# Optimization experiments

Measured on AMD Instinct MI355X. Metric: run time of the kernel, lower is better.

## Reference

```python
import jax, jax.numpy as jnp
import numpy as np


def setup_inputs() -> dict:
    key = jax.random.key(0)
    k1, k2, k3, k4, k5, k6 = jax.random.split(key, 6)
    B, S, I, H = 64, 512, 1024, 1024
    scale_ih = 1.0 / np.sqrt(I)
    scale_hh = 1.0 / np.sqrt(H)
    return {
        "inputs": jax.random.normal(k1, (B, S, I), dtype=jnp.float32),
        "h0": jax.random.normal(k2, (1, B, H), dtype=jnp.float32),
        "weight_ih": jax.random.normal(k3, (H, I), dtype=jnp.float32) * scale_ih,
        "weight_hh": jax.random.normal(k4, (H, H), dtype=jnp.float32) * scale_hh,
        "bias_ih": jax.random.normal(k5, (H,), dtype=jnp.float32) * 0.01,
        "bias_hh": jax.random.normal(k6, (H,), dtype=jnp.float32) * 0.01,
    }


def reference(inputs, h0, weight_ih, weight_hh, bias_ih, bias_hh):
    # Elman RNN with ReLU: h_t = relu(x_t W_ih^T + b_ih + h_{t-1} W_hh^T + b_hh)
    # inputs: [B, S, I]; h0: [1, B, H]
    # Precompute the input projection for all timesteps in one big GEMM.
    x_proj = jnp.einsum('bsi,hi->bsh', inputs, weight_ih) + bias_ih + bias_hh  # [B,S,H]

    def step(h, xp_t):
        h_new = jax.nn.relu(xp_t + jnp.matmul(h, weight_hh.T))  # [B,H]
        return h_new, h_new

    h_init = h0[0]  # [B, H]
    h_last, outs = jax.lax.scan(step, h_init, jnp.swapaxes(x_proj, 0, 1))  # outs: [S,B,H]
    outputs = jnp.swapaxes(outs, 0, 1)  # [B, S, H]
    h_n = h_last[None]  # [1, B, H]
    return outputs, h_n
```

## Files before the change

### kernel.cpp

```cpp
#include <hip/hip_runtime.h>
#include <hip/hip_bf16.h>
#include <stdint.h>

#define BATCH 64
#define SEQ   512
#define INDIM 1024
#define HDIM  1024
#define NBLK  256
#define NGRP  8
#define GSLOT 32
#define FPAD  16
#define HELEMS 32768

typedef short bf16x8 __attribute__((ext_vector_type(8)));
typedef short s16x4  __attribute__((ext_vector_type(4)));
typedef float f32x4  __attribute__((ext_vector_type(4)));
typedef unsigned short u16;
typedef unsigned int   u32;
typedef u32 u32x2 __attribute__((ext_vector_type(2)));
typedef u32 u32x4 __attribute__((ext_vector_type(4)));
typedef u16 u16x4 __attribute__((ext_vector_type(4)));

static __device__ __forceinline__ u16 f2bf(float x) {
  unsigned int u = __float_as_uint(x);
  u += 0x7fffu + ((u >> 16) & 1u);
  return (u16)(u >> 16);
}
static __device__ __forceinline__ float bf2f(u16 b) {
  return __uint_as_float(((unsigned int)b) << 16);
}

static __device__ __forceinline__ int coh_ld_i32(const int* p) {
  int v;
  asm volatile("global_load_dword %0, %1, off sc0 sc1\n\t"
               "s_waitcnt vmcnt(0)"
               : "=&v"(v) : "v"(p) : "memory");
  return v;
}

static __device__ __forceinline__ void split4(float4 v, u16x4& hi, u16x4& lo) {
  hi.x = f2bf(v.x); lo.x = f2bf(v.x - bf2f(hi.x));
  hi.y = f2bf(v.y); lo.y = f2bf(v.y - bf2f(hi.y));
  hi.z = f2bf(v.z); lo.z = f2bf(v.z - bf2f(hi.z));
  hi.w = f2bf(v.w); lo.w = f2bf(v.w - bf2f(hi.w));
}
static __device__ __forceinline__ bf16x8 ld8(const u16* p) {
  s16x4 a = *(const s16x4*)p;
  s16x4 b = *(const s16x4*)(p + 4);
  return __builtin_shufflevector(a, b, 0, 1, 2, 3, 4, 5, 6, 7);
}

__global__ void init0(u32* __restrict__ ws, int n) {
  int i = blockIdx.x * blockDim.x + threadIdx.x;
  if (i < n) ws[i] = 0;
}

__global__ void init1(const float* __restrict__ h0, u16* __restrict__ hbase) {
  int i = blockIdx.x * blockDim.x + threadIdx.x;
  if (i < BATCH * HDIM) {
    int b = i >> 10, k = i & 1023;
    int g = b >> 3, r = b & 7;
    int k32 = k >> 5, kg = (k >> 3) & 3, j = k & 7;
    float x = h0[i];
    u16 h = f2bf(x);
    size_t u = (size_t)(g * 2) * HELEMS + ((size_t)(k32 * 4 + kg) * 16 + r) * 16 + j;
    hbase[u] = h;
    hbase[u + 8] = f2bf(x - bf2f(h));
  }
}

__global__ __launch_bounds__(256) void xproj_kernel(const float* __restrict__ A,
                                                    const float* __restrict__ W,
                                                    const float* __restrict__ bih,
                                                    const float* __restrict__ bhh,
                                                    float* __restrict__ C) {
  __shared__ u16 Ah[4][128][12], Al[4][128][12], Bh[4][128][12], Bl[4][128][12];
  const int nb = blockIdx.x;
  const int mb = blockIdx.y;
  const int m_base = mb * 128, n_base = nb * 128;
  const int tid = (int)threadIdx.x;
  const int wid = tid >> 6, lane = tid & 63;
  const int wm = wid >> 1, wn = wid & 1;
  const int r = lane & 15, kg = lane >> 4;
  const int srow = tid >> 1;
  const int skq  = (tid & 1) * 16;

  const float* ap0 = A + (size_t)(m_base + srow) * INDIM + skq;
  const float* bp0 = W + (size_t)(n_base + srow) * INDIM + skq;

  f32x4 acc[4][4] = {};

  for (int k0 = 0; k0 < INDIM; k0 += 32) {
    float4 av[4], bv[4];
#pragma unroll
    for (int i = 0; i < 4; ++i) {
      av[i] = *(const float4*)(ap0 + k0 + i * 4);
      bv[i] = *(const float4*)(bp0 + k0 + i * 4);
    }
    __syncthreads();
#pragma unroll
    for (int i = 0; i < 4; ++i) {
      int kk = skq + i * 4;
      int kgw = kk >> 3, off = kk & 7;
      u16x4 hi, lo;
      split4(av[i], hi, lo);
      *(u16x4*)&Ah[kgw][srow][off] = hi;
      *(u16x4*)&Al[kgw][srow][off] = lo;
      split4(bv[i], hi, lo);
      *(u16x4*)&Bh[kgw][srow][off] = hi;
      *(u16x4*)&Bl[kgw][srow][off] = lo;
    }
    __syncthreads();

    bf16x8 ah[4], al[4], bhv[4], blv[4];
#pragma unroll
    for (int mf = 0; mf < 4; ++mf) {
      int row = wm * 64 + mf * 16 + r;
      ah[mf] = ld8(&Ah[kg][row][0]);
      al[mf] = ld8(&Al[kg][row][0]);
    }
#pragma unroll
    for (int nf = 0; nf < 4; ++nf) {
      int row = wn * 64 + nf * 16 + r;
      bhv[nf] = ld8(&Bh[kg][row][0]);
      blv[nf] = ld8(&Bl[kg][row][0]);
    }
#pragma unroll
    for (int mf = 0; mf < 4; ++mf)
#pragma unroll
      for (int nf = 0; nf < 4; ++nf) {
        acc[mf][nf] = __builtin_amdgcn_mfma_f32_16x16x32_bf16(ah[mf], bhv[nf], acc[mf][nf], 0, 0, 0);
        acc[mf][nf] = __builtin_amdgcn_mfma_f32_16x16x32_bf16(ah[mf], blv[nf], acc[mf][nf], 0, 0, 0);
        acc[mf][nf] = __builtin_amdgcn_mfma_f32_16x16x32_bf16(al[mf], bhv[nf], acc[mf][nf], 0, 0, 0);
      }
  }

#pragma unroll
  for (int nf = 0; nf < 4; ++nf) {
    int col = n_base + wn * 64 + nf * 16 + r;
    float bias = bih[col] + bhh[col];
#pragma unroll
    for (int mf = 0; mf < 4; ++mf) {
      int rowb = m_base + wm * 64 + mf * 16 + kg * 4;
#pragma unroll
      for (int q = 0; q < 4; ++q) {
        C[(size_t)(rowb + q) * HDIM + col] = acc[mf][nf][q] + bias;
      }
    }
  }
}

__global__ __launch_bounds__(512, 1) void rnn_scan(
    const float* __restrict__ Whh, float* __restrict__ out,
    u16* hbase, int* flags) {
  __shared__ u16 WH[32][2][64][8], WL[32][2][64][8];
  __shared__ __align__(16) float red[2][8][2][8][20];

  const int blk = (int)blockIdx.x;
  const int grp = blk & 7;
  const int slot = blk >> 3;
  const int n0 = slot * 32;
  const int tid = (int)threadIdx.x;
  const int wv = tid >> 6, lane = tid & 63;
  const int r = lane & 15, kg = lane >> 4;

  for (int it = 0; it < 16; ++it) {
    int f4 = it * 512 + tid;
    int row = f4 >> 8;
    int k0 = (f4 & 255) * 4;
    float4 v = *(const float4*)(Whh + (size_t)(n0 + row) * HDIM + k0);
    int k32 = k0 >> 5, kgg = (k0 >> 3) & 3, j = k0 & 7;
    int nt = row >> 4, ln = kgg * 16 + (row & 15);
    u16x4 hi, lo;
    split4(v, hi, lo);
    *(u16x4*)&WH[k32][nt][ln][j] = hi;
    *(u16x4*)&WL[k32][nt][ln][j] = lo;
  }
  __syncthreads();

  u16* const hb[2] = {hbase + (size_t)(grp * 2) * HELEMS,
                      hbase + (size_t)(grp * 2 + 1) * HELEMS};
  int* const gflag = flags + grp * GSLOT * FPAD;
  const bool zrow = (lane & 15) >= 8;
  const int* const pollp = gflag + (wv * 4 + (lane & 3)) * FPAD;

  const int erow = lane >> 3;
  const int ec = lane & 7;
  const float* xp0 = out + ((size_t)(grp * 8 + erow) * SEQ) * HDIM + n0 + ec * 4;
  float4 xf;
  if (wv == 0) xf = *(const float4*)xp0;

  for (int t = 0; t < SEQ; ++t) {
    const int p = t & 1;
    const u16* hc = hb[p];
    u16* hn = hb[p ^ 1];

    if (t > 0) {
      int v;
      do { v = coh_ld_i32(pollp); } while (!__all(v >= t));
    }

    u32x4 hh[4], hl[4];
    if (!zrow) {
      const char* a0 = (const char*)hc + ((size_t)(wv * 4) * 64 + lane) * 32;
      const char* a1 = a0 + 4096;
      asm volatile(
          "global_load_dwordx4 %0, %8, off sc0 sc1\n\t"
          "global_load_dwordx4 %1, %8, off offset:16 sc0 sc1\n\t"
          "global_load_dwordx4 %2, %8, off offset:2048 sc0 sc1\n\t"
          "global_load_dwordx4 %3, %8, off offset:2064 sc0 sc1\n\t"
          "global_load_dwordx4 %4, %9, off sc0 sc1\n\t"
          "global_load_dwordx4 %5, %9, off offset:16 sc0 sc1\n\t"
          "global_load_dwordx4 %6, %9, off offset:2048 sc0 sc1\n\t"
          "global_load_dwordx4 %7, %9, off offset:2064 sc0 sc1"
          : "=&v"(hh[0]), "=&v"(hl[0]), "=&v"(hh[1]), "=&v"(hl[1]),
            "=&v"(hh[2]), "=&v"(hl[2]), "=&v"(hh[3]), "=&v"(hl[3])
          : "v"(a0), "v"(a1)
          : "memory");
      asm volatile("s_waitcnt vmcnt(0)"
          : "+v"(hh[0]), "+v"(hl[0]), "+v"(hh[1]), "+v"(hl[1]),
            "+v"(hh[2]), "+v"(hl[2]), "+v"(hh[3]), "+v"(hl[3]));
    } else {
#pragma unroll
      for (int i = 0; i < 4; ++i) { hh[i] = (u32x4){0,0,0,0}; hl[i] = (u32x4){0,0,0,0}; }
    }

    f32x4 acc0 = {0.f, 0.f, 0.f, 0.f};
    f32x4 acc1 = {0.f, 0.f, 0.f, 0.f};
#pragma unroll
    for (int i = 0; i < 4; ++i) {
      int k32 = wv * 4 + i;
      bf16x8 ah = __builtin_bit_cast(bf16x8, hh[i]);
      bf16x8 al = __builtin_bit_cast(bf16x8, hl[i]);
      bf16x8 b0h = *(const bf16x8*)&WH[k32][0][lane][0];
      bf16x8 b0l = *(const bf16x8*)&WL[k32][0][lane][0];
      bf16x8 b1h = *(const bf16x8*)&WH[k32][1][lane][0];
      bf16x8 b1l = *(const bf16x8*)&WL[k32][1][lane][0];
      acc0 = __builtin_amdgcn_mfma_f32_16x16x32_bf16(ah, b0h, acc0, 0, 0, 0);
      acc0 = __builtin_amdgcn_mfma_f32_16x16x32_bf16(ah, b0l, acc0, 0, 0, 0);
      acc0 = __builtin_amdgcn_mfma_f32_16x16x32_bf16(al, b0h, acc0, 0, 0, 0);
      acc1 = __builtin_amdgcn_mfma_f32_16x16x32_bf16(ah, b1h, acc1, 0, 0, 0);
      acc1 = __builtin_amdgcn_mfma_f32_16x16x32_bf16(ah, b1l, acc1, 0, 0, 0);
      acc1 = __builtin_amdgcn_mfma_f32_16x16x32_bf16(al, b1h, acc1, 0, 0, 0);
    }

    if (kg < 2) {
#pragma unroll
      for (int q = 0; q < 4; ++q) {
        red[p][wv][0][kg * 4 + q][r] = acc0[q];
        red[p][wv][1][kg * 4 + q][r] = acc1[q];
      }
    }
    __syncthreads();

    if (wv == 0) {
      f32x4 s = {xf.x, xf.y, xf.z, xf.w};
      int nt = ec >> 2, cl = (ec & 3) * 4;
#pragma unroll
      for (int w = 0; w < 8; ++w) s += *(const f32x4*)&red[p][w][nt][erow][cl];
#pragma unroll
      for (int j = 0; j < 4; ++j) s[j] = s[j] > 0.f ? s[j] : 0.f;

      union { u16 u[4]; u32x2 d; } HH, LL;
#pragma unroll
      for (int j = 0; j < 4; ++j) {
        u16 h = f2bf(s[j]);
        HH.u[j] = h;
        LL.u[j] = f2bf(s[j] - bf2f(h));
      }
      char* hp = (char*)hn + ((size_t)(slot * 64 + (ec >> 1) * 16 + erow) * 32) + (ec & 1) * 8;
      asm volatile(
          "global_store_dwordx2 %0, %1, off sc0 sc1\n\t"
          "global_store_dwordx2 %0, %2, off offset:16 sc0 sc1\n\t"
          "s_waitcnt vmcnt(0)"
          :: "v"(hp), "v"(HH.d), "v"(LL.d)
          : "memory");
      if (lane == 0) {
        int* fp = gflag + slot * FPAD;
        int tv = t + 1;
        asm volatile("global_store_dword %0, %1, off sc0 sc1"
                     :: "v"(fp), "v"(tv) : "memory");
      }
      __builtin_nontemporal_store(s,
          (f32x4*)(out + ((size_t)(grp * 8 + erow) * SEQ + t) * HDIM + n0 + ec * 4));
      if (t + 1 < SEQ) xf = *(const float4*)(xp0 + (size_t)(t + 1) * HDIM);
    }
  }
}

__global__ void copy_hn(const float* __restrict__ out, float* __restrict__ hn) {
  int idx = blockIdx.x * blockDim.x + threadIdx.x;
  if (idx < BATCH * HDIM) {
    int b = idx >> 10, j = idx & 1023;
    hn[idx] = out[((size_t)b * SEQ + (SEQ - 1)) * (size_t)HDIM + j];
  }
}

extern "C" void kernel_launch(void* const* d_in, const int* in_sizes, int n_in,
                              void* d_out, int out_size, void* d_ws, size_t ws_size,
                              hipStream_t stream) {
  const float* inputs = (const float*)d_in[0];
  const float* h0     = (const float*)d_in[1];
  const float* w_ih   = (const float*)d_in[2];
  const float* w_hh   = (const float*)d_in[3];
  const float* b_ih   = (const float*)d_in[4];
  const float* b_hh   = (const float*)d_in[5];

  float* outBase = (float*)d_out;
  float* hnBase  = outBase + (size_t)BATCH * SEQ * HDIM;

  u16* hbase = (u16*)d_ws;
  int* flags = (int*)(hbase + (size_t)NGRP * 2 * HELEMS);
  const int zero_u32 = (int)(((size_t)NGRP * 2 * HELEMS * 2) / 4 + NGRP * GSLOT * FPAD);

  init0<<<(zero_u32 + 255) / 256, 256, 0, stream>>>((u32*)d_ws, zero_u32);
  init1<<<(BATCH * HDIM + 255) / 256, 256, 0, stream>>>(h0, hbase);

  xproj_kernel<<<dim3(8, 256), 256, 0, stream>>>(inputs, w_ih, b_ih, b_hh, outBase);

  const float* wha = w_hh;
  float* oa = outBase;
  u16* hba = hbase;
  int* fa = flags;
  void* args[4] = {&wha, &oa, &hba, &fa};
  (void)hipLaunchCooperativeKernel((const void*)rnn_scan, dim3(NBLK), dim3(512), args, 0, stream);

  copy_hn<<<256, 256, 0, stream>>>(outBase, hnBase);
}
```

Measured before the change: 1.619 ms.

## Use in-data sign-bit readiness tokens with 4-deep h buffers and 16-row groups

Reorganizes the recurrent scan from 8 groups of 8 batch rows (256 blocks) into 4 groups of 16 rows (128 blocks), so MFMA tiles are no longer half padded with zero rows. Step readiness is now signalled inside the h data itself: the sign bit of the hi bf16 half toggles every 4 steps, and consumers spin on the loaded h values instead of polling flags first. A 4-deep ring buffer replaces double buffering, and the per-block flags are only checked before overwriting a slot to prevent write-after-read hazards. Hi and lo halves are packed into one dword per element, so each thread does a single dwordx4 store. This removes a separate flag round trip from each step's critical path, at the cost of XOR unmasking work and fewer blocks sharing the work.

```diff
diff --git a/kernel.cpp b/kernel.cpp
--- a/kernel.cpp
+++ b/kernel.cpp
@@ -6,18 +6,18 @@
 #define SEQ   512
 #define INDIM 1024
 #define HDIM  1024
-#define NBLK  256
-#define NGRP  8
-#define GSLOT 32
+#define NBLK  128
+#define NPAIR 4
+#define PSLOT 32
+#define DEPTH 4
 #define FPAD  16
-#define HELEMS 32768
+#define PBUF_U16 32768
 
 typedef short bf16x8 __attribute__((ext_vector_type(8)));
 typedef short s16x4  __attribute__((ext_vector_type(4)));
 typedef float f32x4  __attribute__((ext_vector_type(4)));
 typedef unsigned short u16;
 typedef unsigned int   u32;
-typedef u32 u32x2 __attribute__((ext_vector_type(2)));
 typedef u32 u32x4 __attribute__((ext_vector_type(4)));
 typedef u16 u16x4 __attribute__((ext_vector_type(4)));
 
@@ -50,22 +50,24 @@
   return __builtin_shufflevector(a, b, 0, 1, 2, 3, 4, 5, 6, 7);
 }
 
-__global__ void init0(u32* __restrict__ ws, int n) {
+__global__ void init0(u32* __restrict__ ws) {
   int i = blockIdx.x * blockDim.x + threadIdx.x;
-  if (i < n) ws[i] = 0;
-}
-
-__global__ void init1(const float* __restrict__ h0, u16* __restrict__ hbase) {
+  const int hdw = NPAIR * DEPTH * (PBUF_U16 / 2);
+  if (i < hdw) ws[i] = 0xFFFFFFFFu;
+  else if (i < hdw + NPAIR * PSLOT * FPAD) ws[i] = 0;
+}
+
+__global__ void init1(const float* __restrict__ h0, u32* __restrict__ hw) {
   int i = blockIdx.x * blockDim.x + threadIdx.x;
   if (i < BATCH * HDIM) {
     int b = i >> 10, k = i & 1023;
-    int g = b >> 3, r = b & 7;
+    int pp = b >> 4, r = b & 15;
     int k32 = k >> 5, kg = (k >> 3) & 3, j = k & 7;
     float x = h0[i];
-    u16 h = f2bf(x);
-    size_t u = (size_t)(g * 2) * HELEMS + ((size_t)(k32 * 4 + kg) * 16 + r) * 16 + j;
-    hbase[u] = h;
-    hbase[u + 8] = f2bf(x - bf2f(h));
+    u16 hi = f2bf(x);
+    u16 lo = f2bf(x - bf2f(hi));
+    size_t di = (size_t)pp * (DEPTH * PBUF_U16 / 2) + (size_t)((k32 * 64 + kg * 16 + r) * 8 + j);
+    hw[di] = (u32)hi | ((u32)lo << 16);
   }
 }
 
@@ -154,11 +156,11 @@
     const float* __restrict__ Whh, float* __restrict__ out,
     u16* hbase, int* flags) {
   __shared__ u16 WH[32][2][64][8], WL[32][2][64][8];
-  __shared__ __align__(16) float red[2][8][2][8][20];
+  __shared__ float red[2][8][2][16][16];
 
   const int blk = (int)blockIdx.x;
-  const int grp = blk & 7;
-  const int slot = blk >> 3;
+  const int pp = blk & 3;
+  const int slot = blk >> 2;
   const int n0 = slot * 32;
   const int tid = (int)threadIdx.x;
   const int wv = tid >> 6, lane = tid & 63;
@@ -178,111 +180,146 @@
   }
   __syncthreads();
 
-  u16* const hb[2] = {hbase + (size_t)(grp * 2) * HELEMS,
-                      hbase + (size_t)(grp * 2 + 1) * HELEMS};
-  int* const gflag = flags + grp * GSLOT * FPAD;
-  const bool zrow = (lane & 15) >= 8;
-  const int* const pollp = gflag + (wv * 4 + (lane & 3)) * FPAD;
-
-  const int erow = lane >> 3;
+  u16* const hpair = hbase + (size_t)pp * (DEPTH * PBUF_U16);
+  int* const pflag = flags + pp * PSLOT * FPAD;
+
+  const int erow = (wv == 1 ? 8 : 0) + (lane >> 3);
   const int ec = lane & 7;
-  const float* xp0 = out + ((size_t)(grp * 8 + erow) * SEQ) * HDIM + n0 + ec * 4;
+  const float* xp0 = out + ((size_t)(pp * 16 + erow) * SEQ) * HDIM + n0 + ec * 4;
   float4 xf;
-  if (wv == 0) xf = *(const float4*)xp0;
+  if (wv < 2) xf = *(const float4*)xp0;
 
   for (int t = 0; t < SEQ; ++t) {
-    const int p = t & 1;
-    const u16* hc = hb[p];
-    u16* hn = hb[p ^ 1];
-
-    if (t > 0) {
-      int v;
-      do { v = coh_ld_i32(pollp); } while (!__all(v >= t));
-    }
-
-    u32x4 hh[4], hl[4];
-    if (!zrow) {
-      const char* a0 = (const char*)hc + ((size_t)(wv * 4) * 64 + lane) * 32;
+    const int p2 = t & 1;
+    const int rt = (t >> 2) & 1;
+    const u32 rm = rt ? 0x80008000u : 0u;
+    const u16 wm16 = (u16)((((t + 1) >> 2) & 1) << 15);
+    const u16* hc = hpair + (size_t)(t & 3) * PBUF_U16;
+    u16* hn = hpair + (size_t)((t + 1) & 3) * PBUF_U16;
+
+    u32x4 P0, P1, P2, P3, P4, P5, P6, P7;
+    {
+      const char* a0 = (const char*)hc + (size_t)((wv * 4) * 64 + lane) * 32;
       const char* a1 = a0 + 4096;
-      asm volatile(
-          "global_load_dwordx4 %0, %8, off sc0 sc1\n\t"
-          "global_load_dwordx4 %1, %8, off offset:16 sc0 sc1\n\t"
-          "global_load_dwordx4 %2, %8, off offset:2048 sc0 sc1\n\t"
-          "global_load_dwordx4 %3, %8, off offset:2064 sc0 sc1\n\t"
-          "global_load_dwordx4 %4, %9, off sc0 sc1\n\t"
-          "global_load_dwordx4 %5, %9, off offset:16 sc0 sc1\n\t"
-          "global_load_dwordx4 %6, %9, off offset:2048 sc0 sc1\n\t"
-          "global_load_dwordx4 %7, %9, off offset:2064 sc0 sc1"
-          : "=&v"(hh[0]), "=&v"(hl[0]), "=&v"(hh[1]), "=&v"(hl[1]),
-            "=&v"(hh[2]), "=&v"(hl[2]), "=&v"(hh[3]), "=&v"(hl[3])
-          : "v"(a0), "v"(a1)
-          : "memory");
-      asm volatile("s_waitcnt vmcnt(0)"
-          : "+v"(hh[0]), "+v"(hl[0]), "+v"(hh[1]), "+v"(hl[1]),
-            "+v"(hh[2]), "+v"(hl[2]), "+v"(hh[3]), "+v"(hl[3]));
-    } else {
-#pragma unroll
-      for (int i = 0; i < 4; ++i) { hh[i] = (u32x4){0,0,0,0}; hl[i] = (u32x4){0,0,0,0}; }
+      for (;;) {
+        asm volatile(
+            "global_load_dwordx4 %0, %8, off sc0 sc1\n\t"
+            "global_load_dwordx4 %1, %8, off offset:16 sc0 sc1\n\t"
+            "global_load_dwordx4 %2, %8, off offset:2048 sc0 sc1\n\t"
+            "global_load_dwordx4 %3, %8, off offset:2064 sc0 sc1\n\t"
+            "global_load_dwordx4 %4, %9, off sc0 sc1\n\t"
+            "global_load_dwordx4 %5, %9, off offset:16 sc0 sc1\n\t"
+            "global_load_dwordx4 %6, %9, off offset:2048 sc0 sc1\n\t"
+            "global_load_dwordx4 %7, %9, off offset:2064 sc0 sc1"
+            : "=&v"(P0), "=&v"(P1), "=&v"(P2), "=&v"(P3),
+              "=&v"(P4), "=&v"(P5), "=&v"(P6), "=&v"(P7)
+            : "v"(a0), "v"(a1)
+            : "memory");
+        asm volatile("s_waitcnt vmcnt(0)"
+            : "+v"(P0), "+v"(P1), "+v"(P2), "+v"(P3),
+              "+v"(P4), "+v"(P5), "+v"(P6), "+v"(P7));
+        if (t == 0) break;
+        bool okl;
+        if (rt) {
+          u32 m = P0[0] & P0[1] & P0[2] & P0[3] & P1[0] & P1[1] & P1[2] & P1[3]
+                & P2[0] & P2[1] & P2[2] & P2[3] & P3[0] & P3[1] & P3[2] & P3[3]
+                & P4[0] & P4[1] & P4[2] & P4[3] & P5[0] & P5[1] & P5[2] & P5[3]
+                & P6[0] & P6[1] & P6[2] & P6[3] & P7[0] & P7[1] & P7[2] & P7[3];
+          okl = ((m >> 15) & 1u) != 0;
+        } else {
+          u32 m = P0[0] | P0[1] | P0[2] | P0[3] | P1[0] | P1[1] | P1[2] | P1[3]
+                | P2[0] | P2[1] | P2[2] | P2[3] | P3[0] | P3[1] | P3[2] | P3[3]
+                | P4[0] | P4[1] | P4[2] | P4[3] | P5[0] | P5[1] | P5[2] | P5[3]
+                | P6[0] | P6[1] | P6[2] | P6[3] | P7[0] | P7[1] | P7[2] | P7[3];
+          okl = ((m >> 15) & 1u) == 0;
+        }
+        if (__all((int)okl)) break;
+      }
+    }
+
+    int fv = 0;
+    if (wv < 2 && t >= 3) {
+      const int* fp = pflag + (lane & 31) * FPAD;
+      asm volatile("global_load_dword %0, %1, off sc0 sc1"
+                   : "=v"(fv) : "v"(fp) : "memory");
     }
 
     f32x4 acc0 = {0.f, 0.f, 0.f, 0.f};
     f32x4 acc1 = {0.f, 0.f, 0.f, 0.f};
-#pragma unroll
-    for (int i = 0; i < 4; ++i) {
-      int k32 = wv * 4 + i;
-      bf16x8 ah = __builtin_bit_cast(bf16x8, hh[i]);
-      bf16x8 al = __builtin_bit_cast(bf16x8, hl[i]);
-      bf16x8 b0h = *(const bf16x8*)&WH[k32][0][lane][0];
-      bf16x8 b0l = *(const bf16x8*)&WL[k32][0][lane][0];
-      bf16x8 b1h = *(const bf16x8*)&WH[k32][1][lane][0];
-      bf16x8 b1l = *(const bf16x8*)&WL[k32][1][lane][0];
-      acc0 = __builtin_amdgcn_mfma_f32_16x16x32_bf16(ah, b0h, acc0, 0, 0, 0);
-      acc0 = __builtin_amdgcn_mfma_f32_16x16x32_bf16(ah, b0l, acc0, 0, 0, 0);
-      acc0 = __builtin_amdgcn_mfma_f32_16x16x32_bf16(al, b0h, acc0, 0, 0, 0);
-      acc1 = __builtin_amdgcn_mfma_f32_16x16x32_bf16(ah, b1h, acc1, 0, 0, 0);
-      acc1 = __builtin_amdgcn_mfma_f32_16x16x32_bf16(ah, b1l, acc1, 0, 0, 0);
-      acc1 = __builtin_amdgcn_mfma_f32_16x16x32_bf16(al, b1h, acc1, 0, 0, 0);
-    }
-
-    if (kg < 2) {
-#pragma unroll
-      for (int q = 0; q < 4; ++q) {
-        red[p][wv][0][kg * 4 + q][r] = acc0[q];
-        red[p][wv][1][kg * 4 + q][r] = acc1[q];
-      }
+#define DO_K32(i, QA, QB)                                                      \
+    {                                                                          \
+      u32 d0 = QA[0], d1 = QA[1], d2 = QA[2], d3 = QA[3];                      \
+      u32 d4 = QB[0], d5 = QB[1], d6 = QB[2], d7 = QB[3];                      \
+      union { u32 w[4]; bf16x8 v; } AH, AL;                                    \
+      AH.w[0] = ((d0 & 0xFFFFu) | (d1 << 16)) ^ rm;                            \
+      AH.w[1] = ((d2 & 0xFFFFu) | (d3 << 16)) ^ rm;                            \
+      AH.w[2] = ((d4 & 0xFFFFu) | (d5 << 16)) ^ rm;                            \
+      AH.w[3] = ((d6 & 0xFFFFu) | (d7 << 16)) ^ rm;                            \
+      AL.w[0] = (d0 >> 16) | (d1 & 0xFFFF0000u);                               \
+      AL.w[1] = (d2 >> 16) | (d3 & 0xFFFF0000u);                               \
+      AL.w[2] = (d4 >> 16) | (d5 & 0xFFFF0000u);                               \
+      AL.w[3] = (d6 >> 16) | (d7 & 0xFFFF0000u);                               \
+      int k32 = wv * 4 + (i);                                                  \
+      bf16x8 b0h = *(const bf16x8*)&WH[k32][0][lane][0];                       \
+      bf16x8 b0l = *(const bf16x8*)&WL[k32][0][lane][0];                       \
+      bf16x8 b1h = *(const bf16x8*)&WH[k32][1][lane][0];                       \
+      bf16x8 b1l = *(const bf16x8*)&WL[k32][1][lane][0];                       \
+      acc0 = __builtin_amdgcn_mfma_f32_16x16x32_bf16(AH.v, b0h, acc0, 0, 0, 0);\
+      acc0 = __builtin_amdgcn_mfma_f32_16x16x32_bf16(AH.v, b0l, acc0, 0, 0, 0);\
+      acc0 = __builtin_amdgcn_mfma_f32_16x16x32_bf16(AL.v, b0h, acc0, 0, 0, 0);\
+      acc1 = __builtin_amdgcn_mfma_f32_16x16x32_bf16(AH.v, b1h, acc1, 0, 0, 0);\
+      acc1 = __builtin_amdgcn_mfma_f32_16x16x32_bf16(AH.v, b1l, acc1, 0, 0, 0);\
+      acc1 = __builtin_amdgcn_mfma_f32_16x16x32_bf16(AL.v, b1h, acc1, 0, 0, 0);\
+    }
+    DO_K32(0, P0, P1)
+    DO_K32(1, P2, P3)
+    DO_K32(2, P4, P5)
+    DO_K32(3, P6, P7)
+#undef DO_K32
+
+#pragma unroll
+    for (int q = 0; q < 4; ++q) {
+      red[p2][wv][0][kg * 4 + q][r] = acc0[q];
+      red[p2][wv][1][kg * 4 + q][r] = acc1[q];
     }
     __syncthreads();
 
-    if (wv == 0) {
-      f32x4 s = {xf.x, xf.y, xf.z, xf.w};
-      int nt = ec >> 2, cl = (ec & 3) * 4;
-#pragma unroll
-      for (int w = 0; w < 8; ++w) s += *(const f32x4*)&red[p][w][nt][erow][cl];
-#pragma unroll
-      for (int j = 0; j < 4; ++j) s[j] = s[j] > 0.f ? s[j] : 0.f;
-
-      union { u16 u[4]; u32x2 d; } HH, LL;
-#pragma unroll
-      for (int j = 0; j < 4; ++j) {
-        u16 h = f2bf(s[j]);
-        HH.u[j] = h;
-        LL.u[j] = f2bf(s[j] - bf2f(h));
-      }
-      char* hp = (char*)hn + ((size_t)(slot * 64 + (ec >> 1) * 16 + erow) * 32) + (ec & 1) * 8;
-      asm volatile(
-          "global_store_dwordx2 %0, %1, off sc0 sc1\n\t"
-          "global_store_dwordx2 %0, %2, off offset:16 sc0 sc1\n\t"
-          "s_waitcnt vmcnt(0)"
-          :: "v"(hp), "v"(HH.d), "v"(LL.d)
-          : "memory");
-      if (lane == 0) {
-        int* fp = gflag + slot * FPAD;
+    if (wv < 2) {
+      if (wv == 0 && lane == 0) {
+        int* fp = pflag + slot * FPAD;
         int tv = t + 1;
         asm volatile("global_store_dword %0, %1, off sc0 sc1"
                      :: "v"(fp), "v"(tv) : "memory");
       }
+      f32x4 s = {xf.x, xf.y, xf.z, xf.w};
+      int nt = ec >> 2, cl = (ec & 3) * 4;
+#pragma unroll
+      for (int w = 0; w < 8; ++w) s += *(const f32x4*)&red[p2][w][nt][erow][cl];
+#pragma unroll
+      for (int j = 0; j < 4; ++j) s[j] = s[j] > 0.f ? s[j] : 0.f;
+
+      if (t >= 3) {
+        asm volatile("s_waitcnt vmcnt(0)" : "+v"(fv));
+        while (!__all(fv >= t - 2)) fv = coh_ld_i32(pflag + (lane & 31) * FPAD);
+      }
+
+      u32 dw0, dw1, dw2, dw3;
+      {
+        u16 h0 = f2bf(s[0]), h1 = f2bf(s[1]), h2 = f2bf(s[2]), h3 = f2bf(s[3]);
+        u16 l0 = f2bf(s[0] - bf2f(h0)), l1 = f2bf(s[1] - bf2f(h1));
+        u16 l2 = f2bf(s[2] - bf2f(h2)), l3 = f2bf(s[3] - bf2f(h3));
+        dw0 = (u32)(u16)(h0 ^ wm16) | ((u32)l0 << 16);
+        dw1 = (u32)(u16)(h1 ^ wm16) | ((u32)l1 << 16);
+        dw2 = (u32)(u16)(h2 ^ wm16) | ((u32)l2 << 16);
+        dw3 = (u32)(u16)(h3 ^ wm16) | ((u32)l3 << 16);
+      }
+      u32x4 D = {dw0, dw1, dw2, dw3};
+      char* hp = (char*)hn + (size_t)((slot * 64 + (ec >> 1) * 16 + erow) * 32) + (ec & 1) * 16;
+      asm volatile("global_store_dwordx4 %0, %1, off sc0 sc1"
+                   :: "v"(hp), "v"(D) : "memory");
+
       __builtin_nontemporal_store(s,
-          (f32x4*)(out + ((size_t)(grp * 8 + erow) * SEQ + t) * HDIM + n0 + ec * 4));
+          (f32x4*)(out + ((size_t)(pp * 16 + erow) * SEQ + t) * HDIM + n0 + ec * 4));
       if (t + 1 < SEQ) xf = *(const float4*)(xp0 + (size_t)(t + 1) * HDIM);
     }
   }
@@ -310,11 +347,11 @@
   float* hnBase  = outBase + (size_t)BATCH * SEQ * HDIM;
 
   u16* hbase = (u16*)d_ws;
-  int* flags = (int*)(hbase + (size_t)NGRP * 2 * HELEMS);
-  const int zero_u32 = (int)(((size_t)NGRP * 2 * HELEMS * 2) / 4 + NGRP * GSLOT * FPAD);
-
-  init0<<<(zero_u32 + 255) / 256, 256, 0, stream>>>((u32*)d_ws, zero_u32);
-  init1<<<(BATCH * HDIM + 255) / 256, 256, 0, stream>>>(h0, hbase);
+  int* flags = (int*)(hbase + (size_t)NPAIR * DEPTH * PBUF_U16);
+
+  const int init_n = NPAIR * DEPTH * (PBUF_U16 / 2) + NPAIR * PSLOT * FPAD;
+  init0<<<(init_n + 255) / 256, 256, 0, stream>>>((u32*)d_ws);
+  init1<<<(BATCH * HDIM + 255) / 256, 256, 0, stream>>>(h0, (u32*)hbase);
 
   xproj_kernel<<<dim3(8, 256), 256, 0, stream>>>(inputs, w_ih, b_ih, b_hh, outBase);
 
```

Result: slower. 2.331 ms (+44.0%).
